# Kernel optimization log

Hardware: AMD Instinct MI355X
Metric: run time of the kernel (lower is better)

## Reference

```python
import jax, jax.numpy as jnp
import numpy as np

B = 2097152  # number of Gaussians


def setup_inputs() -> dict:
    key = jax.random.key(0)
    k1, k2, k3, k4, k5, k6 = jax.random.split(key, 6)
    return {
        "loc1": jax.random.normal(k1, (B, 3), dtype=jnp.float32),
        "scale1": jax.random.uniform(k2, (B, 3), dtype=jnp.float32),
        "rot_matrix1": jax.random.normal(k3, (B, 3, 3), dtype=jnp.float32),
        "loc2": jax.random.normal(k4, (B, 3), dtype=jnp.float32),
        "scale2": jax.random.uniform(k5, (B, 3), dtype=jnp.float32),
        "rot_matrix2": jax.random.normal(k6, (B, 3, 3), dtype=jnp.float32),
    }


def reference(loc1, scale1, rot_matrix1, loc2, scale2, rot_matrix2):
    # ||mu1 - mu2||^2  -> (B,)
    loc_diff2 = jnp.sum((loc1 - loc2) ** 2, axis=-1)

    # cov2 = R2 diag(scale2) R2^T  -> (B,3,3)
    cov2 = jnp.einsum("bij,bj,bkj->bik", rot_matrix2, scale2, rot_matrix2)
    # cov2 rotated into frame of Gaussian 1: R1^T cov2 R1  -> (B,3,3)
    cov2_R1 = jnp.einsum("bji,bjk,bkl->bil", rot_matrix1, cov2, rot_matrix1)

    # E = diag(sqrt(s1)) cov2_R1 diag(sqrt(s1)), then symmetrize
    s1_sqrt = jnp.sqrt(scale1)  # (B,3)
    E = s1_sqrt[:, :, None] * cov2_R1 * s1_sqrt[:, None, :]
    E = (E + jnp.swapaxes(E, 1, 2)) * 0.5

    # trace of matrix sqrt via eigenvalues: sum (lambda^2)^(1/4) = sum |lambda|^(1/2)
    E_eig = jnp.linalg.eigvalsh(E)  # (B,3)
    E_sqrt_trace = jnp.sum(jnp.sqrt(jnp.sqrt(E_eig ** 2)), axis=-1)

    cov_wasserstein = jnp.sum(scale1, axis=-1) + jnp.sum(scale2, axis=-1) - 2.0 * E_sqrt_trace
    cov_wasserstein = jnp.maximum(cov_wasserstein, 0.0)
    return jnp.sqrt(loc_diff2 + cov_wasserstein)
```

## Files before the change

kernel.cpp:

```cpp
#include <hip/hip_runtime.h>
#include <math.h>

#define BLK 256

__global__ __launch_bounds__(BLK) void wasserstein_kernel(
    const float* __restrict__ loc1,   const float* __restrict__ scale1,
    const float* __restrict__ rot1,   const float* __restrict__ loc2,
    const float* __restrict__ scale2, const float* __restrict__ rot2,
    float* __restrict__ out)
{
    __shared__ float smem[BLK * 30];
    float* sL1 = smem;
    float* sS1 = smem + BLK * 3;
    float* sR1 = smem + BLK * 6;
    float* sL2 = smem + BLK * 15;
    float* sS2 = smem + BLK * 18;
    float* sR2 = smem + BLK * 21;

    const int tid = threadIdx.x;
    const long long blockStart = (long long)blockIdx.x * BLK;

    {
        const float4* g4;
        float4* l4;

        g4 = reinterpret_cast<const float4*>(loc1 + blockStart * 3);
        l4 = reinterpret_cast<float4*>(sL1);
        for (int i = tid; i < BLK * 3 / 4; i += BLK) l4[i] = g4[i];

        g4 = reinterpret_cast<const float4*>(scale1 + blockStart * 3);
        l4 = reinterpret_cast<float4*>(sS1);
        for (int i = tid; i < BLK * 3 / 4; i += BLK) l4[i] = g4[i];

        g4 = reinterpret_cast<const float4*>(rot1 + blockStart * 9);
        l4 = reinterpret_cast<float4*>(sR1);
        for (int i = tid; i < BLK * 9 / 4; i += BLK) l4[i] = g4[i];

        g4 = reinterpret_cast<const float4*>(loc2 + blockStart * 3);
        l4 = reinterpret_cast<float4*>(sL2);
        for (int i = tid; i < BLK * 3 / 4; i += BLK) l4[i] = g4[i];

        g4 = reinterpret_cast<const float4*>(scale2 + blockStart * 3);
        l4 = reinterpret_cast<float4*>(sS2);
        for (int i = tid; i < BLK * 3 / 4; i += BLK) l4[i] = g4[i];

        g4 = reinterpret_cast<const float4*>(rot2 + blockStart * 9);
        l4 = reinterpret_cast<float4*>(sR2);
        for (int i = tid; i < BLK * 9 / 4; i += BLK) l4[i] = g4[i];
    }
    __syncthreads();

    const float l1x = sL1[tid * 3 + 0], l1y = sL1[tid * 3 + 1], l1z = sL1[tid * 3 + 2];
    const float l2x = sL2[tid * 3 + 0], l2y = sL2[tid * 3 + 1], l2z = sL2[tid * 3 + 2];
    const float dx = l1x - l2x, dy = l1y - l2y, dz = l1z - l2z;
    const float loc_diff2 = dx * dx + dy * dy + dz * dz;

    const float s1a = sS1[tid * 3 + 0], s1b = sS1[tid * 3 + 1], s1c = sS1[tid * 3 + 2];
    const float s2a = sS2[tid * 3 + 0], s2b = sS2[tid * 3 + 1], s2c = sS2[tid * 3 + 2];

    float R1[9], R2[9];
#pragma unroll
    for (int k = 0; k < 9; ++k) R1[k] = sR1[tid * 9 + k];
#pragma unroll
    for (int k = 0; k < 9; ++k) R2[k] = sR2[tid * 9 + k];

    const float m00 = s2a * R2[0] * R2[0] + s2b * R2[1] * R2[1] + s2c * R2[2] * R2[2];
    const float m01 = s2a * R2[0] * R2[3] + s2b * R2[1] * R2[4] + s2c * R2[2] * R2[5];
    const float m02 = s2a * R2[0] * R2[6] + s2b * R2[1] * R2[7] + s2c * R2[2] * R2[8];
    const float m11 = s2a * R2[3] * R2[3] + s2b * R2[4] * R2[4] + s2c * R2[5] * R2[5];
    const float m12 = s2a * R2[3] * R2[6] + s2b * R2[4] * R2[7] + s2c * R2[5] * R2[8];
    const float m22 = s2a * R2[6] * R2[6] + s2b * R2[7] * R2[7] + s2c * R2[8] * R2[8];

    float A[9];
    A[0] = m00 * R1[0] + m01 * R1[3] + m02 * R1[6];
    A[1] = m00 * R1[1] + m01 * R1[4] + m02 * R1[7];
    A[2] = m00 * R1[2] + m01 * R1[5] + m02 * R1[8];
    A[3] = m01 * R1[0] + m11 * R1[3] + m12 * R1[6];
    A[4] = m01 * R1[1] + m11 * R1[4] + m12 * R1[7];
    A[5] = m01 * R1[2] + m11 * R1[5] + m12 * R1[8];
    A[6] = m02 * R1[0] + m12 * R1[3] + m22 * R1[6];
    A[7] = m02 * R1[1] + m12 * R1[4] + m22 * R1[7];
    A[8] = m02 * R1[2] + m12 * R1[5] + m22 * R1[8];

    float T[9];
    T[0] = R1[0] * A[0] + R1[3] * A[3] + R1[6] * A[6];
    T[1] = R1[0] * A[1] + R1[3] * A[4] + R1[6] * A[7];
    T[2] = R1[0] * A[2] + R1[3] * A[5] + R1[6] * A[8];
    T[3] = R1[1] * A[0] + R1[4] * A[3] + R1[7] * A[6];
    T[4] = R1[1] * A[1] + R1[4] * A[4] + R1[7] * A[7];
    T[5] = R1[1] * A[2] + R1[4] * A[5] + R1[7] * A[8];
    T[6] = R1[2] * A[0] + R1[5] * A[3] + R1[8] * A[6];
    T[7] = R1[2] * A[1] + R1[5] * A[4] + R1[8] * A[7];
    T[8] = R1[2] * A[2] + R1[5] * A[5] + R1[8] * A[8];

    const float sq0 = sqrtf(s1a), sq1 = sqrtf(s1b), sq2 = sqrtf(s1c);
    const float e00 = s1a * T[0];
    const float e11 = s1b * T[4];
    const float e22 = s1c * T[8];
    const float e01 = 0.5f * sq0 * sq1 * (T[1] + T[3]);
    const float e02 = 0.5f * sq0 * sq2 * (T[2] + T[6]);
    const float e12 = 0.5f * sq1 * sq2 * (T[5] + T[7]);

    const float q  = (e00 + e11 + e22) * (1.0f / 3.0f);
    const float p1 = e01 * e01 + e02 * e02 + e12 * e12;
    const float d0 = e00 - q, d1 = e11 - q, d2 = e22 - q;
    const float p2 = d0 * d0 + d1 * d1 + d2 * d2 + 2.0f * p1;

    float trace_sqrt;
    if (p2 > 1e-24f) {
        const float p   = sqrtf(p2 * (1.0f / 6.0f));
        const float inv = 1.0f / p;
        const float b00 = d0 * inv, b11 = d1 * inv, b22 = d2 * inv;
        const float b01 = e01 * inv, b02 = e02 * inv, b12 = e12 * inv;
        float detB = b00 * (b11 * b22 - b12 * b12)
                   - b01 * (b01 * b22 - b12 * b02)
                   + b02 * (b01 * b12 - b11 * b02);
        float r = 0.5f * detB;
        r = fminf(fmaxf(r, -1.0f), 1.0f);
        const float phi  = acosf(r) * (1.0f / 3.0f);
        const float twop = 2.0f * p;
        const float eig1 = q + twop * cosf(phi);
        const float eig3 = q + twop * cosf(phi + 2.0943951023931953f);
        const float eig2 = 3.0f * q - eig1 - eig3;
        trace_sqrt = sqrtf(fabsf(eig1)) + sqrtf(fabsf(eig2)) + sqrtf(fabsf(eig3));
    } else {
        trace_sqrt = 3.0f * sqrtf(fabsf(q));
    }

    float cov_w = (s1a + s1b + s1c) + (s2a + s2b + s2c) - 2.0f * trace_sqrt;
    cov_w = fmaxf(cov_w, 0.0f);
    out[blockStart + tid] = sqrtf(loc_diff2 + cov_w);
}

extern "C" void kernel_launch(void* const* d_in, const int* in_sizes, int n_in,
                              void* d_out, int out_size, void* d_ws, size_t ws_size,
                              hipStream_t stream) {
    const float* loc1   = (const float*)d_in[0];
    const float* scale1 = (const float*)d_in[1];
    const float* rot1   = (const float*)d_in[2];
    const float* loc2   = (const float*)d_in[3];
    const float* scale2 = (const float*)d_in[4];
    const float* rot2   = (const float*)d_in[5];
    float* out = (float*)d_out;

    const int B = in_sizes[0] / 3;
    const int grid = B / BLK;

    wasserstein_kernel<<<grid, BLK, 0, stream>>>(loc1, scale1, rot1,
                                                 loc2, scale2, rot2, out);
}
```

Baseline: 240.7 us.

## Stage rotation matrices via per-wave global_load_lds DMA and load loc/scale directly

The kernel no longer stages all six inputs through shared memory with float4 copies and a block-wide barrier. Only the two rotation matrices are staged, per wave, using the direct global-to-LDS load builtin, and each wave waits on its own vmcnt instead of calling __syncthreads. Locations and scales are read straight into registers as 12-byte structs. Launch bounds now request 8 blocks per CU. The goal is less LDS traffic and footprint and no block-level synchronisation, at the cost of relying on the hand-written waitcnt for correct ordering and on unaligned 12-byte global loads.

```diff
diff --git a/kernel.cpp b/kernel.cpp
--- a/kernel.cpp
+++ b/kernel.cpp
@@ -3,66 +3,65 @@
 
 #define BLK 256
 
-__global__ __launch_bounds__(BLK) void wasserstein_kernel(
+typedef __attribute__((address_space(1))) void gvoid_t;
+typedef __attribute__((address_space(3))) void lvoid_t;
+
+__device__ __forceinline__ void lds_dma16(const float* gsrc, float* ldst) {
+    __builtin_amdgcn_global_load_lds((gvoid_t*)gsrc, (lvoid_t*)ldst, 16, 0, 0);
+}
+__device__ __forceinline__ void lds_dma4(const float* gsrc, float* ldst) {
+    __builtin_amdgcn_global_load_lds((gvoid_t*)gsrc, (lvoid_t*)ldst, 4, 0, 0);
+}
+
+struct F3 { float x, y, z; };
+
+__global__ __launch_bounds__(BLK, 8) void wasserstein_kernel(
     const float* __restrict__ loc1,   const float* __restrict__ scale1,
     const float* __restrict__ rot1,   const float* __restrict__ loc2,
     const float* __restrict__ scale2, const float* __restrict__ rot2,
     float* __restrict__ out)
 {
-    __shared__ float smem[BLK * 30];
-    float* sL1 = smem;
-    float* sS1 = smem + BLK * 3;
-    float* sR1 = smem + BLK * 6;
-    float* sL2 = smem + BLK * 15;
-    float* sS2 = smem + BLK * 18;
-    float* sR2 = smem + BLK * 21;
+    __shared__ __align__(16) float smem[4 * 1152];
 
-    const int tid = threadIdx.x;
+    const int tid  = threadIdx.x;
+    const int lane = tid & 63;
+    const int wave = tid >> 6;
     const long long blockStart = (long long)blockIdx.x * BLK;
+    const long long waveStart  = blockStart + (long long)(wave * 64);
+
+    float* wR1 = smem + wave * 1152;
+    float* wR2 = wR1 + 576;
 
     {
-        const float4* g4;
-        float4* l4;
+        const float* g1 = rot1 + waveStart * 9;
+        const float* g2 = rot2 + waveStart * 9;
+        lds_dma16(g1 + lane * 4,       wR1);
+        lds_dma16(g1 + 256 + lane * 4, wR1 + 256);
+        lds_dma4 (g1 + 512 + lane,     wR1 + 512);
+        lds_dma16(g2 + lane * 4,       wR2);
+        lds_dma16(g2 + 256 + lane * 4, wR2 + 256);
+        lds_dma4 (g2 + 512 + lane,     wR2 + 512);
+    }
 
-        g4 = reinterpret_cast<const float4*>(loc1 + blockStart * 3);
-        l4 = reinterpret_cast<float4*>(sL1);
-        for (int i = tid; i < BLK * 3 / 4; i += BLK) l4[i] = g4[i];
+    const long long i = blockStart + tid;
+    const F3 L1 = *reinterpret_cast<const F3*>(loc1   + i * 3);
+    const F3 L2 = *reinterpret_cast<const F3*>(loc2   + i * 3);
+    const F3 S1 = *reinterpret_cast<const F3*>(scale1 + i * 3);
+    const F3 S2 = *reinterpret_cast<const F3*>(scale2 + i * 3);
 
-        g4 = reinterpret_cast<const float4*>(scale1 + blockStart * 3);
-        l4 = reinterpret_cast<float4*>(sS1);
-        for (int i = tid; i < BLK * 3 / 4; i += BLK) l4[i] = g4[i];
+    const float dx = L1.x - L2.x, dy = L1.y - L2.y, dz = L1.z - L2.z;
+    const float loc_diff2 = dx * dx + dy * dy + dz * dz;
+    const float s1a = S1.x, s1b = S1.y, s1c = S1.z;
+    const float s2a = S2.x, s2b = S2.y, s2c = S2.z;
 
-        g4 = reinterpret_cast<const float4*>(rot1 + blockStart * 9);
-        l4 = reinterpret_cast<float4*>(sR1);
-        for (int i = tid; i < BLK * 9 / 4; i += BLK) l4[i] = g4[i];
-
-        g4 = reinterpret_cast<const float4*>(loc2 + blockStart * 3);
-        l4 = reinterpret_cast<float4*>(sL2);
-        for (int i = tid; i < BLK * 3 / 4; i += BLK) l4[i] = g4[i];
-
-        g4 = reinterpret_cast<const float4*>(scale2 + blockStart * 3);
-        l4 = reinterpret_cast<float4*>(sS2);
-        for (int i = tid; i < BLK * 3 / 4; i += BLK) l4[i] = g4[i];
-
-        g4 = reinterpret_cast<const float4*>(rot2 + blockStart * 9);
-        l4 = reinterpret_cast<float4*>(sR2);
-        for (int i = tid; i < BLK * 9 / 4; i += BLK) l4[i] = g4[i];
-    }
-    __syncthreads();
-
-    const float l1x = sL1[tid * 3 + 0], l1y = sL1[tid * 3 + 1], l1z = sL1[tid * 3 + 2];
-    const float l2x = sL2[tid * 3 + 0], l2y = sL2[tid * 3 + 1], l2z = sL2[tid * 3 + 2];
-    const float dx = l1x - l2x, dy = l1y - l2y, dz = l1z - l2z;
-    const float loc_diff2 = dx * dx + dy * dy + dz * dz;
-
-    const float s1a = sS1[tid * 3 + 0], s1b = sS1[tid * 3 + 1], s1c = sS1[tid * 3 + 2];
-    const float s2a = sS2[tid * 3 + 0], s2b = sS2[tid * 3 + 1], s2c = sS2[tid * 3 + 2];
+    asm volatile("s_waitcnt vmcnt(0)" ::: "memory");
+    __builtin_amdgcn_sched_barrier(0);
 
     float R1[9], R2[9];
 #pragma unroll
-    for (int k = 0; k < 9; ++k) R1[k] = sR1[tid * 9 + k];
+    for (int k = 0; k < 9; ++k) R1[k] = wR1[lane * 9 + k];
 #pragma unroll
-    for (int k = 0; k < 9; ++k) R2[k] = sR2[tid * 9 + k];
+    for (int k = 0; k < 9; ++k) R2[k] = wR2[lane * 9 + k];
 
     const float m00 = s2a * R2[0] * R2[0] + s2b * R2[1] * R2[1] + s2c * R2[2] * R2[2];
     const float m01 = s2a * R2[0] * R2[3] + s2b * R2[1] * R2[4] + s2c * R2[2] * R2[5];
@@ -129,7 +128,7 @@
 
     float cov_w = (s1a + s1b + s1c) + (s2a + s2b + s2c) - 2.0f * trace_sqrt;
     cov_w = fmaxf(cov_w, 0.0f);
-    out[blockStart + tid] = sqrtf(loc_diff2 + cov_w);
+    out[i] = sqrtf(loc_diff2 + cov_w);
 }
 
 extern "C" void kernel_launch(void* const* d_in, const int* in_sizes, int n_in,
```

After: 238.7 us. No clear change (-0.8%).
